# Optimization experiments

Hardware: AMD Instinct MI355X
Metric: run time of the kernel (lower is better)

The kernel has to match this reference:

```python
import jax, jax.numpy as jnp
import numpy as np


def setup_inputs() -> dict:
    key = jax.random.key(0)
    ks = jax.random.split(key, 5)
    B, C, H, W = 4, 256, 64, 64
    Cq = C // 8
    x = jax.random.normal(ks[0], (B, C, H, W), dtype=jnp.float32)
    Wq = jax.random.normal(ks[1], (Cq, C), dtype=jnp.float32) * (1.0 / np.sqrt(C))
    Wk = jax.random.normal(ks[2], (Cq, C), dtype=jnp.float32) * (1.0 / np.sqrt(C))
    Wv = jax.random.normal(ks[3], (C, C), dtype=jnp.float32) * (1.0 / np.sqrt(C))
    bq = jnp.zeros((Cq,), dtype=jnp.float32)
    bk = jnp.zeros((Cq,), dtype=jnp.float32)
    bv = jnp.zeros((C,), dtype=jnp.float32)
    gamma = jnp.ones((1,), dtype=jnp.float32)
    return {"x": x, "Wq": Wq, "bq": bq, "Wk": Wk, "bk": bk, "Wv": Wv, "bv": bv, "gamma": gamma}


def reference(x, Wq, bq, Wk, bk, Wv, bv, gamma):
    B, C, H, W = x.shape
    N = H * W
    xf = x.reshape(B, C, N)                      # (B, C, N)
    # 1x1 convs == per-pixel linear projections over channels
    q = jnp.einsum('dc,bcn->bdn', Wq, xf) + bq[None, :, None]   # (B, C/8, N)
    k = jnp.einsum('dc,bcn->bdn', Wk, xf) + bk[None, :, None]   # (B, C/8, N)
    v = jnp.einsum('dc,bcn->bdn', Wv, xf) + bv[None, :, None]   # (B, C,   N)
    # attention: note original has NO 1/sqrt(d) scaling
    scores = jnp.einsum('bdn,bdm->bnm', q, k)     # (B, N, N)
    attn = jax.nn.softmax(scores, axis=-1)
    out = jnp.einsum('bnm,bdm->bnd', attn, v)     # (B, N, C)
    out = out.transpose(0, 2, 1).reshape(B, C, H, W)
    return gamma * out + x
```

## Files before the change

### kernel.cpp

```cpp
#include <hip/hip_runtime.h>

#define BATCH 4
#define CH    256
#define DQ    32
#define NPIX  4096

typedef unsigned short u16;
typedef unsigned int   u32;
typedef __attribute__((ext_vector_type(8))) short short8;
typedef __attribute__((ext_vector_type(16))) float f32x16;

__device__ __forceinline__ float b2f(u32 u) {
  union { u32 i; float f; } v; v.i = (u & 0xffffu) << 16; return v.f;
}
__device__ __forceinline__ u16 f2b(float f) {
  union { float f; u32 i; } v; v.f = f;
  u32 x = v.i; x += 0x7fffu + ((x >> 16) & 1u);
  return (u16)(x >> 16);
}

__global__ __launch_bounds__(256) void wconv(
    const float* __restrict__ Wq, const float* __restrict__ Wk,
    const float* __restrict__ Wv, u16* __restrict__ wsz, u16* __restrict__ wsz_lo)
{
  const int blk = blockIdx.x;
  const int jt = blk >> 4, kk = blk & 15;
  #pragma unroll
  for (int rep = 0; rep < 2; ++rep) {
    const int idx = rep * 256 + threadIdx.x;
    const int j = idx >> 4, el = idx & 15, e = kk * 16 + el;
    const float* Wsrc = (jt == 0) ? Wq : (jt == 1) ? Wk : Wv;
    const int row = (jt <= 1) ? j : (jt - 2) * 32 + j;
    const float v = Wsrc[(size_t)row * CH + e];
    const u16 hi = f2b(v);
    const int o = (((jt * 16 + kk) * 2 + (el >> 3)) * 32 + j) * 8 + (el & 7);
    wsz[o] = hi;
    if (jt < 2) wsz_lo[o] = f2b(v - b2f(hi));
  }
}

__global__ __launch_bounds__(512, 2) void proj(
    const float* __restrict__ x,
    const u16* __restrict__ wsz, const u16* __restrict__ wsz_lo,
    const float* __restrict__ bq, const float* __restrict__ bk, const float* __restrict__ bv,
    u16* __restrict__ q_t, u16* __restrict__ k_t, u16* __restrict__ v_swz)
{
  const int b = blockIdx.y, nt = blockIdx.x;
  const int n0 = nt * 32;
  const int t = threadIdx.x;
  const int w = t >> 6, lane = t & 63, hl = lane >> 5, l31 = lane & 31;

  __shared__ __align__(16) u16 xh[32 * 264];
  __shared__ __align__(16) u16 xl[32 * 264];

  #pragma unroll
  for (int i = 0; i < 4; ++i) {
    const int e = i * 64 + (t >> 3), n4 = t & 7;
    const float4 v4 = *(const float4*)&x[((size_t)b * CH + e) * NPIX + n0 + n4 * 4];
    const float vv[4] = {v4.x, v4.y, v4.z, v4.w};
    #pragma unroll
    for (int jj = 0; jj < 4; ++jj) {
      const u16 hi = f2b(vv[jj]);
      xh[(n4 * 4 + jj) * 264 + e] = hi;
      xl[(n4 * 4 + jj) * 264 + e] = f2b(vv[jj] - b2f(hi));
    }
  }
  __syncthreads();

  const int cnt[8] = {1, 1, 1, 1, 2, 2, 1, 1};
  const int j0a[8] = {0, 1, 2, 4, 6, 8, 3, 5};
  const int j1a[8] = {-1, -1, -1, -1, 7, 9, -1, -1};

  for (int ii = 0; ii < cnt[w]; ++ii) {
    const int jt = (ii == 0) ? j0a[w] : j1a[w];
    f32x16 acc;
    #pragma unroll
    for (int r = 0; r < 16; ++r) acc[r] = 0.f;

    if (jt <= 1) {
      #pragma unroll
      for (int kk = 0; kk < 16; ++kk) {
        const int wo = ((jt * 16 + kk) * 2 + hl) * 256 + l31 * 8;
        const short8 Ah = *(const short8*)&wsz[wo];
        const short8 Al = *(const short8*)&wsz_lo[wo];
        const int xo = l31 * 264 + kk * 16 + hl * 8;
        const short8 Bh = *(const short8*)&xh[xo];
        const short8 Bl = *(const short8*)&xl[xo];
        acc = __builtin_amdgcn_mfma_f32_32x32x16_bf16(Ah, Bh, acc, 0, 0, 0);
        acc = __builtin_amdgcn_mfma_f32_32x32x16_bf16(Ah, Bl, acc, 0, 0, 0);
        acc = __builtin_amdgcn_mfma_f32_32x32x16_bf16(Al, Bh, acc, 0, 0, 0);
      }
    } else {
      #pragma unroll
      for (int kk = 0; kk < 16; ++kk) {
        const short8 Ah = *(const short8*)&wsz[((jt * 16 + kk) * 2 + hl) * 256 + l31 * 8];
        const short8 Bh = *(const short8*)&xh[l31 * 264 + kk * 16 + hl * 8];
        acc = __builtin_amdgcn_mfma_f32_32x32x16_bf16(Ah, Bh, acc, 0, 0, 0);
      }
    }

    if (jt <= 1) {
      u16* dst = (jt == 0) ? q_t : k_t;
      const float* bias = (jt == 0) ? bq : bk;
      const int n = n0 + l31;
      #pragma unroll
      for (int r = 0; r < 16; ++r) {
        const int d = (r & 3) + 8 * (r >> 2) + 4 * hl;
        dst[((size_t)b * NPIX + n) * DQ + d] = f2b(acc[r] + bias[d]);
      }
    } else {
      const int ctv = jt - 2;
      const int kc = (l31 >> 4) & 1, h3 = (l31 >> 3) & 1, j8 = l31 & 7;
      const size_t base = ((((size_t)b * 128 + nt) * 8 + ctv) * 2 + kc) * 2 + h3;
      #pragma unroll
      for (int r = 0; r < 16; ++r) {
        const int c5 = (r & 3) + 8 * (r >> 2) + 4 * hl;
        v_swz[base * 256 + c5 * 8 + j8] = f2b(acc[r] + bv[ctv * 32 + c5]);
      }
    }
  }
}

__global__ __launch_bounds__(512, 2) void attn(
    const u16* __restrict__ q_t, const u16* __restrict__ k_t,
    const u16* __restrict__ v_swz, const float* __restrict__ x,
    const float* __restrict__ gamma, float* __restrict__ out)
{
  const int b = blockIdx.y, t = threadIdx.x;
  const int w = t >> 6, lane = t & 63, hl = lane >> 5, l31 = lane & 31;
  const int mq = w & 3, ch = w >> 2;
  const int n0 = blockIdx.x * 64;

  __shared__ __align__(16) char smem[32768 + 2048];
  uint4* plds = (uint4*)smem;
  float* cbuf = (float*)smem;
  float* lbuf = (float*)(smem + 32768);

  short8 qf[2];
  #pragma unroll
  for (int kd = 0; kd < 2; ++kd)
    qf[kd] = *(const short8*)(q_t + ((size_t)b * NPIX + n0 + ch * 32 + l31) * DQ + kd * 16 + hl * 8);

  f32x16 acc[8];
  #pragma unroll
  for (int a = 0; a < 8; ++a)
    #pragma unroll
    for (int r = 0; r < 16; ++r) acc[a][r] = 0.f;
  float lrun = 0.f;

  for (int cc = 0; cc < 32; ++cc) {
    const int mc = mq * 32 + cc;

    const u16* kp = k_t + ((size_t)b * NPIX + mc * 32 + l31) * DQ + hl * 8;
    const short8 kf0 = *(const short8*)(kp);
    const short8 kf1 = *(const short8*)(kp + 16);
    f32x16 st;
    #pragma unroll
    for (int r = 0; r < 16; ++r) st[r] = 0.f;
    st = __builtin_amdgcn_mfma_f32_32x32x16_bf16(kf0, qf[0], st, 0, 0, 0);
    st = __builtin_amdgcn_mfma_f32_32x32x16_bf16(kf1, qf[1], st, 0, 0, 0);

    u32 pk[4][2];
    #pragma unroll
    for (int g = 0; g < 4; ++g) {
      const float e0 = __expf(st[4 * g + 0]);
      const float e1 = __expf(st[4 * g + 1]);
      const float e2 = __expf(st[4 * g + 2]);
      const float e3 = __expf(st[4 * g + 3]);
      lrun += (e0 + e1) + (e2 + e3);
      pk[g][0] = (u32)f2b(e0) | ((u32)f2b(e1) << 16);
      pk[g][1] = (u32)f2b(e2) | ((u32)f2b(e3) << 16);
    }

    uint4 bown[2];
    #pragma unroll
    for (int kc = 0; kc < 2; ++kc) {
      const u32 s0 = hl ? pk[2 * kc][0] : pk[2 * kc + 1][0];
      const u32 s1 = hl ? pk[2 * kc][1] : pk[2 * kc + 1][1];
      const u32 r0 = (u32)__shfl_xor((int)s0, 32);
      const u32 r1 = (u32)__shfl_xor((int)s1, 32);
      bown[kc].x = hl ? r0 : pk[2 * kc][0];
      bown[kc].y = hl ? r1 : pk[2 * kc][1];
      bown[kc].z = hl ? pk[2 * kc + 1][0] : r0;
      bown[kc].w = hl ? pk[2 * kc + 1][1] : r1;
    }

    short8 av[4][2];
    const size_t vbase = ((size_t)b * 128 + mc) * 8192;
    #pragma unroll
    for (int ct = 0; ct < 4; ++ct)
      #pragma unroll
      for (int kc = 0; kc < 2; ++kc)
        av[ct][kc] = *(const short8*)(v_swz + vbase +
                       (size_t)((((ch * 4 + ct) * 2 + kc) * 2 + hl) * 256 + l31 * 8));

    const int buf = cc & 1;
    plds[(((buf * 4 + mq) * 2 + ch) * 2 + 0) * 64 + lane] = bown[0];
    plds[(((buf * 4 + mq) * 2 + ch) * 2 + 1) * 64 + lane] = bown[1];
    __syncthreads();
    union { uint4 u; short8 s; } bu[2][2];
    #pragma unroll
    for (int nt = 0; nt < 2; ++nt)
      #pragma unroll
      for (int kc = 0; kc < 2; ++kc)
        bu[nt][kc].u = plds[(((buf * 4 + mq) * 2 + nt) * 2 + kc) * 64 + lane];

    #pragma unroll
    for (int kc = 0; kc < 2; ++kc)
      #pragma unroll
      for (int ct = 0; ct < 4; ++ct)
        #pragma unroll
        for (int nt = 0; nt < 2; ++nt)
          acc[nt * 4 + ct] =
            __builtin_amdgcn_mfma_f32_32x32x16_bf16(av[ct][kc], bu[nt][kc].s, acc[nt * 4 + ct], 0, 0, 0);
  }

  lbuf[w * 64 + lane] = lrun;
  __syncthreads();

  const int srcs[3] = {1, 3, 2}, dsts[3] = {0, 2, 0};
  #pragma unroll
  for (int h = 0; h < 2; ++h) {
    for (int rnd = 0; rnd < 3; ++rnd) {
      if (mq == srcs[rnd]) {
        #pragma unroll
        for (int ct = 0; ct < 4; ++ct)
          #pragma unroll
          for (int r = 0; r < 16; ++r)
            cbuf[ch * 4096 + (ct * 16 + r) * 64 + lane] = acc[h * 4 + ct][r];
      }
      __syncthreads();
      if (mq == dsts[rnd]) {
        #pragma unroll
        for (int ct = 0; ct < 4; ++ct)
          #pragma unroll
          for (int r = 0; r < 16; ++r)
            acc[h * 4 + ct][r] += cbuf[ch * 4096 + (ct * 16 + r) * 64 + lane];
      }
      __syncthreads();
    }
  }

  if (mq == 0) {
    float linv[2];
    #pragma unroll
    for (int nt = 0; nt < 2; ++nt) {
      float l = (lbuf[(nt * 4 + 0) * 64 + lane] + lbuf[(nt * 4 + 1) * 64 + lane])
              + (lbuf[(nt * 4 + 2) * 64 + lane] + lbuf[(nt * 4 + 3) * 64 + lane]);
      l += __shfl_xor(l, 32);
      linv[nt] = 1.0f / l;
    }
    const float g = gamma[0];
    #pragma unroll
    for (int nt = 0; nt < 2; ++nt)
      #pragma unroll
      for (int ct = 0; ct < 4; ++ct)
        #pragma unroll
        for (int r = 0; r < 16; ++r) {
          const int c = (ch * 4 + ct) * 32 + (r & 3) + 8 * (r >> 2) + 4 * hl;
          const size_t idx = ((size_t)b * CH + c) * NPIX + n0 + nt * 32 + l31;
          out[idx] = g * acc[nt * 4 + ct][r] * linv[nt] + x[idx];
        }
  }
}

extern "C" void kernel_launch(void* const* d_in, const int* in_sizes, int n_in,
                              void* d_out, int out_size, void* d_ws, size_t ws_size,
                              hipStream_t stream) {
  const float* x  = (const float*)d_in[0];
  const float* Wq = (const float*)d_in[1];
  const float* bq = (const float*)d_in[2];
  const float* Wk = (const float*)d_in[3];
  const float* bk = (const float*)d_in[4];
  const float* Wv = (const float*)d_in[5];
  const float* bv = (const float*)d_in[6];
  const float* gm = (const float*)d_in[7];
  float* out = (float*)d_out;

  const size_t qk_e = (size_t)BATCH * NPIX * DQ;
  const size_t v_e  = (size_t)BATCH * NPIX * CH;
  const size_t w_e  = 10 * 16 * 2 * 32 * 8;
  const size_t wl_e = 2 * 16 * 2 * 32 * 8;
  const size_t need = (2 * qk_e + v_e + w_e + wl_e) * sizeof(u16);
  if (ws_size < need) return;

  u16* q_t    = (u16*)d_ws;
  u16* k_t    = q_t + qk_e;
  u16* v_swz  = k_t + qk_e;
  u16* wsz    = v_swz + v_e;
  u16* wsz_lo = wsz + w_e;

  wconv<<<dim3(160), 256, 0, stream>>>(Wq, Wk, Wv, wsz, wsz_lo);
  proj <<<dim3(NPIX / 32, BATCH), 512, 0, stream>>>(x, wsz, wsz_lo, bq, bk, bv, q_t, k_t, v_swz);
  attn <<<dim3(NPIX / 64, BATCH), 512, 0, stream>>>(q_t, k_t, v_swz, x, gm, out);
}
```

Before: 185.0 us.

## Fold log2e into Wq for exp2, drop LDS P-exchange, split proj per tile

Scales Wq (and bq) by log2e so the softmax can use a native exp2 instead of expf, and packs bf16 via a byte-permute truncation instead of round-to-nearest. The attention kernel now has each wave compute scores for both query sub-tiles itself, which removes the per-iteration LDS store, __syncthreads and reload of P at the cost of redundant QK MFMAs and exps. The reduction tree is restructured for the new wave mapping. The projection kernel becomes one 64-thread block per output tile reading x directly from global memory with strided loads, dropping its LDS staging and giving more blocks.

Measured after the change: 182.9 us. About the same (-1.1%).

```diff
diff --git a/kernel.cpp b/kernel.cpp
--- a/kernel.cpp
+++ b/kernel.cpp
@@ -4,12 +4,23 @@
 #define CH    256
 #define DQ    32
 #define NPIX  4096
+#define LOG2E 1.4426950408889634f
 
 typedef unsigned short u16;
 typedef unsigned int   u32;
 typedef __attribute__((ext_vector_type(8))) short short8;
 typedef __attribute__((ext_vector_type(16))) float f32x16;
 
+#if defined(__has_builtin)
+#if __has_builtin(__builtin_amdgcn_exp2f)
+#define EXP2F(x) __builtin_amdgcn_exp2f(x)
+#else
+#define EXP2F(x) __expf((x) * 0.6931471805599453f)
+#endif
+#else
+#define EXP2F(x) __expf((x) * 0.6931471805599453f)
+#endif
+
 __device__ __forceinline__ float b2f(u32 u) {
   union { u32 i; float f; } v; v.i = (u & 0xffffu) << 16; return v.f;
 }
@@ -17,6 +28,10 @@
   union { float f; u32 i; } v; v.f = f;
   u32 x = v.i; x += 0x7fffu + ((x >> 16) & 1u);
   return (u16)(x >> 16);
+}
+__device__ __forceinline__ u32 pack_hi16(float lo, float hi) {
+  union { float f; u32 i; } a, b; a.f = lo; b.f = hi;
+  return __builtin_amdgcn_perm(b.i, a.i, 0x07060302u);
 }
 
 __global__ __launch_bounds__(256) void wconv(
@@ -31,7 +46,8 @@
     const int j = idx >> 4, el = idx & 15, e = kk * 16 + el;
     const float* Wsrc = (jt == 0) ? Wq : (jt == 1) ? Wk : Wv;
     const int row = (jt <= 1) ? j : (jt - 2) * 32 + j;
-    const float v = Wsrc[(size_t)row * CH + e];
+    float v = Wsrc[(size_t)row * CH + e];
+    if (jt == 0) v *= LOG2E;
     const u16 hi = f2b(v);
     const int o = (((jt * 16 + kk) * 2 + (el >> 3)) * 32 + j) * 8 + (el & 7);
     wsz[o] = hi;
@@ -39,84 +55,72 @@
   }
 }
 
-__global__ __launch_bounds__(512, 2) void proj(
+__global__ __launch_bounds__(64, 4) void proj(
     const float* __restrict__ x,
     const u16* __restrict__ wsz, const u16* __restrict__ wsz_lo,
     const float* __restrict__ bq, const float* __restrict__ bk, const float* __restrict__ bv,
     u16* __restrict__ q_t, u16* __restrict__ k_t, u16* __restrict__ v_swz)
 {
-  const int b = blockIdx.y, nt = blockIdx.x;
-  const int n0 = nt * 32;
-  const int t = threadIdx.x;
-  const int w = t >> 6, lane = t & 63, hl = lane >> 5, l31 = lane & 31;
-
-  __shared__ __align__(16) u16 xh[32 * 264];
-  __shared__ __align__(16) u16 xl[32 * 264];
-
-  #pragma unroll
-  for (int i = 0; i < 4; ++i) {
-    const int e = i * 64 + (t >> 3), n4 = t & 7;
-    const float4 v4 = *(const float4*)&x[((size_t)b * CH + e) * NPIX + n0 + n4 * 4];
-    const float vv[4] = {v4.x, v4.y, v4.z, v4.w};
-    #pragma unroll
-    for (int jj = 0; jj < 4; ++jj) {
-      const u16 hi = f2b(vv[jj]);
-      xh[(n4 * 4 + jj) * 264 + e] = hi;
-      xl[(n4 * 4 + jj) * 264 + e] = f2b(vv[jj] - b2f(hi));
-    }
-  }
-  __syncthreads();
-
-  const int cnt[8] = {1, 1, 1, 1, 2, 2, 1, 1};
-  const int j0a[8] = {0, 1, 2, 4, 6, 8, 3, 5};
-  const int j1a[8] = {-1, -1, -1, -1, 7, 9, -1, -1};
-
-  for (int ii = 0; ii < cnt[w]; ++ii) {
-    const int jt = (ii == 0) ? j0a[w] : j1a[w];
-    f32x16 acc;
-    #pragma unroll
-    for (int r = 0; r < 16; ++r) acc[r] = 0.f;
-
-    if (jt <= 1) {
-      #pragma unroll
-      for (int kk = 0; kk < 16; ++kk) {
-        const int wo = ((jt * 16 + kk) * 2 + hl) * 256 + l31 * 8;
-        const short8 Ah = *(const short8*)&wsz[wo];
-        const short8 Al = *(const short8*)&wsz_lo[wo];
-        const int xo = l31 * 264 + kk * 16 + hl * 8;
-        const short8 Bh = *(const short8*)&xh[xo];
-        const short8 Bl = *(const short8*)&xl[xo];
-        acc = __builtin_amdgcn_mfma_f32_32x32x16_bf16(Ah, Bh, acc, 0, 0, 0);
-        acc = __builtin_amdgcn_mfma_f32_32x32x16_bf16(Ah, Bl, acc, 0, 0, 0);
-        acc = __builtin_amdgcn_mfma_f32_32x32x16_bf16(Al, Bh, acc, 0, 0, 0);
+  const int nt = blockIdx.x, jt = blockIdx.y, b = blockIdx.z;
+  const int lane = threadIdx.x & 63, hl = lane >> 5, l31 = lane & 31;
+  const int n = nt * 32 + l31;
+
+  f32x16 acc;
+  #pragma unroll
+  for (int r = 0; r < 16; ++r) acc[r] = 0.f;
+
+  const float* xb = x + (size_t)b * CH * NPIX + n;
+
+  if (jt <= 1) {
+    for (int kk = 0; kk < 16; ++kk) {
+      const int wo = ((jt * 16 + kk) * 2 + hl) * 256 + l31 * 8;
+      const short8 Ah = *(const short8*)&wsz[wo];
+      const short8 Al = *(const short8*)&wsz_lo[wo];
+      float xv[8];
+      #pragma unroll
+      for (int j = 0; j < 8; ++j)
+        xv[j] = xb[(size_t)(kk * 16 + hl * 8 + j) * NPIX];
+      union { u32 u[4]; short8 s; } Bh, Bl;
+      #pragma unroll
+      for (int j2 = 0; j2 < 4; ++j2) {
+        const u16 h0 = f2b(xv[2 * j2]),     h1 = f2b(xv[2 * j2 + 1]);
+        const u16 l0 = f2b(xv[2 * j2] - b2f(h0));
+        const u16 l1 = f2b(xv[2 * j2 + 1] - b2f(h1));
+        Bh.u[j2] = (u32)h0 | ((u32)h1 << 16);
+        Bl.u[j2] = (u32)l0 | ((u32)l1 << 16);
       }
-    } else {
-      #pragma unroll
-      for (int kk = 0; kk < 16; ++kk) {
-        const short8 Ah = *(const short8*)&wsz[((jt * 16 + kk) * 2 + hl) * 256 + l31 * 8];
-        const short8 Bh = *(const short8*)&xh[l31 * 264 + kk * 16 + hl * 8];
-        acc = __builtin_amdgcn_mfma_f32_32x32x16_bf16(Ah, Bh, acc, 0, 0, 0);
-      }
-    }
-
-    if (jt <= 1) {
-      u16* dst = (jt == 0) ? q_t : k_t;
-      const float* bias = (jt == 0) ? bq : bk;
-      const int n = n0 + l31;
-      #pragma unroll
-      for (int r = 0; r < 16; ++r) {
-        const int d = (r & 3) + 8 * (r >> 2) + 4 * hl;
-        dst[((size_t)b * NPIX + n) * DQ + d] = f2b(acc[r] + bias[d]);
-      }
-    } else {
-      const int ctv = jt - 2;
-      const int kc = (l31 >> 4) & 1, h3 = (l31 >> 3) & 1, j8 = l31 & 7;
-      const size_t base = ((((size_t)b * 128 + nt) * 8 + ctv) * 2 + kc) * 2 + h3;
-      #pragma unroll
-      for (int r = 0; r < 16; ++r) {
-        const int c5 = (r & 3) + 8 * (r >> 2) + 4 * hl;
-        v_swz[base * 256 + c5 * 8 + j8] = f2b(acc[r] + bv[ctv * 32 + c5]);
-      }
+      acc = __builtin_amdgcn_mfma_f32_32x32x16_bf16(Ah, Bh.s, acc, 0, 0, 0);
+      acc = __builtin_amdgcn_mfma_f32_32x32x16_bf16(Ah, Bl.s, acc, 0, 0, 0);
+      acc = __builtin_amdgcn_mfma_f32_32x32x16_bf16(Al, Bh.s, acc, 0, 0, 0);
+    }
+    u16* dst = (jt == 0) ? q_t : k_t;
+    const float* bias = (jt == 0) ? bq : bk;
+    const float bscale = (jt == 0) ? LOG2E : 1.0f;
+    #pragma unroll
+    for (int r = 0; r < 16; ++r) {
+      const int d = (r & 3) + 8 * (r >> 2) + 4 * hl;
+      dst[((size_t)b * NPIX + n) * DQ + d] = f2b(acc[r] + bias[d] * bscale);
+    }
+  } else {
+    for (int kk = 0; kk < 16; ++kk) {
+      const short8 Ah = *(const short8*)&wsz[((jt * 16 + kk) * 2 + hl) * 256 + l31 * 8];
+      float xv[8];
+      #pragma unroll
+      for (int j = 0; j < 8; ++j)
+        xv[j] = xb[(size_t)(kk * 16 + hl * 8 + j) * NPIX];
+      union { u32 u[4]; short8 s; } Bh;
+      #pragma unroll
+      for (int j2 = 0; j2 < 4; ++j2)
+        Bh.u[j2] = (u32)f2b(xv[2 * j2]) | ((u32)f2b(xv[2 * j2 + 1]) << 16);
+      acc = __builtin_amdgcn_mfma_f32_32x32x16_bf16(Ah, Bh.s, acc, 0, 0, 0);
+    }
+    const int ctv = jt - 2;
+    const int kc = (l31 >> 4) & 1, h3 = (l31 >> 3) & 1, j8 = l31 & 7;
+    u16* dst = v_swz + (((((size_t)b * 128 + nt) * 8 + ctv) * 2 + kc) * 2 + h3) * 256 + j8;
+    #pragma unroll
+    for (int r = 0; r < 16; ++r) {
+      const int c5 = (r & 3) + 8 * (r >> 2) + 4 * hl;
+      dst[c5 * 8] = f2b(acc[r] + bv[ctv * 32 + c5]);
     }
   }
 }
@@ -128,82 +132,75 @@
 {
   const int b = blockIdx.y, t = threadIdx.x;
   const int w = t >> 6, lane = t & 63, hl = lane >> 5, l31 = lane & 31;
-  const int mq = w & 3, ch = w >> 2;
+  const int mq = w >> 1, ch = w & 1;
   const int n0 = blockIdx.x * 64;
 
-  __shared__ __align__(16) char smem[32768 + 2048];
-  uint4* plds = (uint4*)smem;
-  float* cbuf = (float*)smem;
-  float* lbuf = (float*)(smem + 32768);
-
-  short8 qf[2];
-  #pragma unroll
-  for (int kd = 0; kd < 2; ++kd)
-    qf[kd] = *(const short8*)(q_t + ((size_t)b * NPIX + n0 + ch * 32 + l31) * DQ + kd * 16 + hl * 8);
+  __shared__ float cbuf[16384];
+  __shared__ float lbuf[8][2][64];
+
+  short8 qf[2][2];
+  #pragma unroll
+  for (int nt = 0; nt < 2; ++nt)
+    #pragma unroll
+    for (int kd = 0; kd < 2; ++kd)
+      qf[nt][kd] = *(const short8*)(q_t + ((size_t)b * NPIX + n0 + nt * 32 + l31) * DQ + kd * 16 + hl * 8);
 
   f32x16 acc[8];
   #pragma unroll
   for (int a = 0; a < 8; ++a)
     #pragma unroll
     for (int r = 0; r < 16; ++r) acc[a][r] = 0.f;
-  float lrun = 0.f;
+  float lrun[2] = {0.f, 0.f};
+
+  const u16* kb = k_t + (size_t)b * NPIX * DQ;
+  const u16* vb = v_swz + (size_t)b * 128 * 8192;
 
   for (int cc = 0; cc < 32; ++cc) {
     const int mc = mq * 32 + cc;
 
-    const u16* kp = k_t + ((size_t)b * NPIX + mc * 32 + l31) * DQ + hl * 8;
+    const u16* kp = kb + (size_t)(mc * 32 + l31) * DQ + hl * 8;
     const short8 kf0 = *(const short8*)(kp);
     const short8 kf1 = *(const short8*)(kp + 16);
-    f32x16 st;
-    #pragma unroll
-    for (int r = 0; r < 16; ++r) st[r] = 0.f;
-    st = __builtin_amdgcn_mfma_f32_32x32x16_bf16(kf0, qf[0], st, 0, 0, 0);
-    st = __builtin_amdgcn_mfma_f32_32x32x16_bf16(kf1, qf[1], st, 0, 0, 0);
-
-    u32 pk[4][2];
-    #pragma unroll
-    for (int g = 0; g < 4; ++g) {
-      const float e0 = __expf(st[4 * g + 0]);
-      const float e1 = __expf(st[4 * g + 1]);
-      const float e2 = __expf(st[4 * g + 2]);
-      const float e3 = __expf(st[4 * g + 3]);
-      lrun += (e0 + e1) + (e2 + e3);
-      pk[g][0] = (u32)f2b(e0) | ((u32)f2b(e1) << 16);
-      pk[g][1] = (u32)f2b(e2) | ((u32)f2b(e3) << 16);
-    }
-
-    uint4 bown[2];
-    #pragma unroll
-    for (int kc = 0; kc < 2; ++kc) {
-      const u32 s0 = hl ? pk[2 * kc][0] : pk[2 * kc + 1][0];
-      const u32 s1 = hl ? pk[2 * kc][1] : pk[2 * kc + 1][1];
-      const u32 r0 = (u32)__shfl_xor((int)s0, 32);
-      const u32 r1 = (u32)__shfl_xor((int)s1, 32);
-      bown[kc].x = hl ? r0 : pk[2 * kc][0];
-      bown[kc].y = hl ? r1 : pk[2 * kc][1];
-      bown[kc].z = hl ? pk[2 * kc + 1][0] : r0;
-      bown[kc].w = hl ? pk[2 * kc + 1][1] : r1;
-    }
 
     short8 av[4][2];
-    const size_t vbase = ((size_t)b * 128 + mc) * 8192;
+    const u16* vp = vb + (size_t)mc * 8192 + (size_t)hl * 256 + l31 * 8;
     #pragma unroll
     for (int ct = 0; ct < 4; ++ct)
       #pragma unroll
       for (int kc = 0; kc < 2; ++kc)
-        av[ct][kc] = *(const short8*)(v_swz + vbase +
-                       (size_t)((((ch * 4 + ct) * 2 + kc) * 2 + hl) * 256 + l31 * 8));
-
-    const int buf = cc & 1;
-    plds[(((buf * 4 + mq) * 2 + ch) * 2 + 0) * 64 + lane] = bown[0];
-    plds[(((buf * 4 + mq) * 2 + ch) * 2 + 1) * 64 + lane] = bown[1];
-    __syncthreads();
+        av[ct][kc] = *(const short8*)(vp + (((ch * 4 + ct) * 2 + kc) * 2) * 256);
+
     union { uint4 u; short8 s; } bu[2][2];
     #pragma unroll
-    for (int nt = 0; nt < 2; ++nt)
-      #pragma unroll
-      for (int kc = 0; kc < 2; ++kc)
-        bu[nt][kc].u = plds[(((buf * 4 + mq) * 2 + nt) * 2 + kc) * 64 + lane];
+    for (int nt = 0; nt < 2; ++nt) {
+      f32x16 st;
+      #pragma unroll
+      for (int r = 0; r < 16; ++r) st[r] = 0.f;
+      st = __builtin_amdgcn_mfma_f32_32x32x16_bf16(kf0, qf[nt][0], st, 0, 0, 0);
+      st = __builtin_amdgcn_mfma_f32_32x32x16_bf16(kf1, qf[nt][1], st, 0, 0, 0);
+      u32 pk[4][2];
+      #pragma unroll
+      for (int g = 0; g < 4; ++g) {
+        const float e0 = EXP2F(st[4 * g + 0]);
+        const float e1 = EXP2F(st[4 * g + 1]);
+        const float e2 = EXP2F(st[4 * g + 2]);
+        const float e3 = EXP2F(st[4 * g + 3]);
+        lrun[nt] += (e0 + e1) + (e2 + e3);
+        pk[g][0] = pack_hi16(e0, e1);
+        pk[g][1] = pack_hi16(e2, e3);
+      }
+      #pragma unroll
+      for (int kc = 0; kc < 2; ++kc) {
+        const u32 s0 = hl ? pk[2 * kc][0] : pk[2 * kc + 1][0];
+        const u32 s1 = hl ? pk[2 * kc][1] : pk[2 * kc + 1][1];
+        const u32 r0 = (u32)__shfl_xor((int)s0, 32);
+        const u32 r1 = (u32)__shfl_xor((int)s1, 32);
+        bu[nt][kc].u.x = hl ? r0 : pk[2 * kc][0];
+        bu[nt][kc].u.y = hl ? r1 : pk[2 * kc][1];
+        bu[nt][kc].u.z = hl ? pk[2 * kc + 1][0] : r0;
+        bu[nt][kc].u.w = hl ? pk[2 * kc + 1][1] : r1;
+      }
+    }
 
     #pragma unroll
     for (int kc = 0; kc < 2; ++kc)
@@ -215,52 +212,67 @@
             __builtin_amdgcn_mfma_f32_32x32x16_bf16(av[ct][kc], bu[nt][kc].s, acc[nt * 4 + ct], 0, 0, 0);
   }
 
-  lbuf[w * 64 + lane] = lrun;
-  __syncthreads();
-
-  const int srcs[3] = {1, 3, 2}, dsts[3] = {0, 2, 0};
-  #pragma unroll
-  for (int h = 0; h < 2; ++h) {
-    for (int rnd = 0; rnd < 3; ++rnd) {
-      if (mq == srcs[rnd]) {
-        #pragma unroll
-        for (int ct = 0; ct < 4; ++ct)
-          #pragma unroll
-          for (int r = 0; r < 16; ++r)
-            cbuf[ch * 4096 + (ct * 16 + r) * 64 + lane] = acc[h * 4 + ct][r];
-      }
-      __syncthreads();
-      if (mq == dsts[rnd]) {
-        #pragma unroll
-        for (int ct = 0; ct < 4; ++ct)
-          #pragma unroll
-          for (int r = 0; r < 16; ++r)
-            acc[h * 4 + ct][r] += cbuf[ch * 4096 + (ct * 16 + r) * 64 + lane];
-      }
-      __syncthreads();
-    }
+  lbuf[w][0][lane] = lrun[0];
+  lbuf[w][1][lane] = lrun[1];
+
+  #pragma unroll
+  for (int nt = 0; nt < 2; ++nt) {
+    if (mq == 1 || mq == 3) {
+      const int slot = (ch * 2 + (mq >> 1)) * 4096;
+      #pragma unroll
+      for (int ct = 0; ct < 4; ++ct)
+        #pragma unroll
+        for (int r = 0; r < 16; ++r)
+          cbuf[slot + (ct * 16 + r) * 64 + lane] = acc[nt * 4 + ct][r];
+    }
+    __syncthreads();
+    if (mq == 0 || mq == 2) {
+      const int slot = (ch * 2 + (mq >> 1)) * 4096;
+      #pragma unroll
+      for (int ct = 0; ct < 4; ++ct)
+        #pragma unroll
+        for (int r = 0; r < 16; ++r)
+          acc[nt * 4 + ct][r] += cbuf[slot + (ct * 16 + r) * 64 + lane];
+    }
+    __syncthreads();
+    if (mq == 2) {
+      const int slot = ch * 2 * 4096;
+      #pragma unroll
+      for (int ct = 0; ct < 4; ++ct)
+        #pragma unroll
+        for (int r = 0; r < 16; ++r)
+          cbuf[slot + (ct * 16 + r) * 64 + lane] = acc[nt * 4 + ct][r];
+    }
+    __syncthreads();
+    if (mq == 0) {
+      const int slot = ch * 2 * 4096;
+      #pragma unroll
+      for (int ct = 0; ct < 4; ++ct)
+        #pragma unroll
+        for (int r = 0; r < 16; ++r)
+          acc[nt * 4 + ct][r] += cbuf[slot + (ct * 16 + r) * 64 + lane];
+    }
+    __syncthreads();
   }
 
   if (mq == 0) {
-    float linv[2];
+    const float g = gamma[0];
     #pragma unroll
     for (int nt = 0; nt < 2; ++nt) {
-      float l = (lbuf[(nt * 4 + 0) * 64 + lane] + lbuf[(nt * 4 + 1) * 64 + lane])
-              + (lbuf[(nt * 4 + 2) * 64 + lane] + lbuf[(nt * 4 + 3) * 64 + lane]);
+      float l = 0.f;
+      #pragma unroll
+      for (int ww = 0; ww < 8; ++ww) l += lbuf[ww][nt][lane];
       l += __shfl_xor(l, 32);
-      linv[nt] = 1.0f / l;
-    }
-    const float g = gamma[0];
-    #pragma unroll
-    for (int nt = 0; nt < 2; ++nt)
+      const float linv = 2.0f / l;
       #pragma unroll
       for (int ct = 0; ct < 4; ++ct)
         #pragma unroll
         for (int r = 0; r < 16; ++r) {
           const int c = (ch * 4 + ct) * 32 + (r & 3) + 8 * (r >> 2) + 4 * hl;
           const size_t idx = ((size_t)b * CH + c) * NPIX + n0 + nt * 32 + l31;
-          out[idx] = g * acc[nt * 4 + ct][r] * linv[nt] + x[idx];
+          out[idx] = g * acc[nt * 4 + ct][r] * linv + x[idx];
         }
+    }
   }
 }
 
@@ -291,6 +303,6 @@
   u16* wsz_lo = wsz + w_e;
 
   wconv<<<dim3(160), 256, 0, stream>>>(Wq, Wk, Wv, wsz, wsz_lo);
-  proj <<<dim3(NPIX / 32, BATCH), 512, 0, stream>>>(x, wsz, wsz_lo, bq, bk, bv, q_t, k_t, v_swz);
+  proj <<<dim3(NPIX / 32, 10, BATCH), 64, 0, stream>>>(x, wsz, wsz_lo, bq, bk, bv, q_t, k_t, v_swz);
   attn <<<dim3(NPIX / 64, BATCH), 512, 0, stream>>>(q_t, k_t, v_swz, x, gm, out);
 }
```
